# Kernel tuning notes

Hardware: AMD Instinct MI355X
Metric: run time of the kernel (lower is better)

The kernel has to match this reference:

```python
import jax, jax.numpy as jnp
import numpy as np

B, L, HID, H, D = 2, 2048, 1024, 16, 64
ROPE_BASE = 10000.0


def half_rotate(x):
    # [a, b | c, d] -> [-c, -d | a, b] along last dim
    d = x.shape[-1] // 2
    return jnp.concatenate((-x[..., d:], x[..., :d]), axis=-1)


def apply_rope(x, position_ids, base=ROPE_BASE):
    # x: [B, L, H, D]; position_ids: [L] int
    dim = x.shape[-1]
    inv_fre = 1.0 / (base ** (jnp.arange(0, dim, 2, dtype=jnp.float32) / dim))  # [D/2]
    freqs = position_ids.astype(jnp.float32)[None, :, None] * inv_fre  # [1, L, D/2]
    sin = jnp.repeat(jnp.sin(freqs), 2, axis=-1)[:, :, None, :]  # [1, L, 1, D]
    cos = jnp.repeat(jnp.cos(freqs), 2, axis=-1)[:, :, None, :]
    return cos * x + half_rotate(x) * sin


def setup_inputs() -> dict:
    key = jax.random.key(0)
    ks = jax.random.split(key, 5)
    x = jax.random.normal(ks[0], (B, L, HID), dtype=jnp.float32)
    position_id = jnp.arange(L, dtype=jnp.int64)
    # additive causal mask: 0 on/below diagonal, -1e9 above
    causal = jnp.tril(jnp.ones((L, L), dtype=bool))
    atten_mask = jnp.where(causal, 0.0, -1e9).astype(jnp.float32)[None, None]
    s = 1.0 / np.sqrt(HID)
    Wq = jax.random.normal(ks[1], (HID, H * D), dtype=jnp.float32) * s
    Wk = jax.random.normal(ks[2], (HID, H * D), dtype=jnp.float32) * s
    Wv = jax.random.normal(ks[3], (HID, H * D), dtype=jnp.float32) * s
    Wo = jax.random.normal(ks[4], (H * D, HID), dtype=jnp.float32) * s
    return {"x": x, "position_id": position_id, "atten_mask": atten_mask,
            "Wq": Wq, "Wk": Wk, "Wv": Wv, "Wo": Wo}


def reference(x, position_id, atten_mask, Wq, Wk, Wv, Wo):
    b, l, _ = x.shape
    scale = D ** -0.5
    q = (x @ Wq).reshape(b, l, H, D)
    k = (x @ Wk).reshape(b, l, H, D)
    v = (x @ Wv).reshape(b, l, H, D)
    q = apply_rope(q, position_id)
    k = apply_rope(k, position_id)
    # [B, H, Lq, Lk]
    scores = jnp.einsum('bqhd,bkhd->bhqk', q, k) * scale + atten_mask
    attn = jax.nn.softmax(scores.astype(jnp.float32), axis=-1).astype(q.dtype)
    out = jnp.einsum('bhqk,bkhd->bqhd', attn, v).reshape(b, l, H * D)
    return out @ Wo
```

## Files before the change

### kernel.cpp

```cpp
#include <hip/hip_runtime.h>

typedef unsigned short u16;
typedef unsigned int u32;
typedef __attribute__((ext_vector_type(8))) short short8;
typedef __attribute__((ext_vector_type(4))) float f32x4;

#define H_ 16
#define L_ 2048
#define D_ 64
#define HID_ 1024

__device__ __forceinline__ u16 f2bf(float f) {
  union { float f; u32 u; } v; v.f = f;
  u32 r = v.u + 0x7FFFu + ((v.u >> 16) & 1u);
  return (u16)(r >> 16);
}

__device__ __forceinline__ void gl16(const u16* g, u16* l) {
  __builtin_amdgcn_global_load_lds(
      (const __attribute__((address_space(1))) void*)g,
      (__attribute__((address_space(3))) void*)l, 16, 0, 0);
}


__global__ __launch_bounds__(256) void prep_k(
    const float* __restrict__ x, u16* __restrict__ xbf,
    const float* __restrict__ Wq, const float* __restrict__ Wk,
    const float* __restrict__ Wv, const float* __restrict__ Wo,
    u16* __restrict__ dWq, u16* __restrict__ dWk,
    u16* __restrict__ dWv, u16* __restrict__ dWo,
    const int* __restrict__ pos, float2* __restrict__ tab)
{
  __shared__ float t[32][33];
  int blk = blockIdx.x;
  if (blk < 2048) {
    int i = (blk * 256 + threadIdx.x) * 8;
    float4 a = *(const float4*)(x + i);
    float4 b = *(const float4*)(x + i + 4);
    u16 r[8] = { f2bf(a.x), f2bf(a.y), f2bf(a.z), f2bf(a.w),
                 f2bf(b.x), f2bf(b.y), f2bf(b.z), f2bf(b.w) };
    *(uint4*)(xbf + i) = *(const uint4*)r;
  } else if (blk < 6144) {
    int bb = blk - 2048;
    int w = bb >> 10;
    const float* in = (w == 0) ? Wq : (w == 1) ? Wk : (w == 2) ? Wv : Wo;
    u16* out = (w == 0) ? dWq : (w == 1) ? dWk : (w == 2) ? dWv : dWo;
    int bx = bb & 31, by = (bb >> 5) & 31;
    int c = threadIdx.x & 31, r0 = threadIdx.x >> 5;
#pragma unroll
    for (int p = 0; p < 4; ++p) {
      int r = r0 + p * 8;
      t[r][c] = in[(size_t)(by * 32 + r) * 1024 + bx * 32 + c];
    }
    __syncthreads();
#pragma unroll
    for (int p = 0; p < 4; ++p) {
      int r = r0 + p * 8;
      out[(size_t)(bx * 32 + r) * 1024 + by * 32 + c] = f2bf(t[c][r]);
    }
  } else {
    int gid = (blk - 6144) * 256 + threadIdx.x;
    int l = gid >> 5, i = gid & 31;
    float p = (float)pos[l];
    float inv = expf(-((float)(2 * i) / 64.0f) * logf(10000.0f));
    float th = p * inv;
    tab[gid] = make_float2(cosf(th), sinf(th));
  }
}


__global__ __launch_bounds__(256) void qkv_gemm_k(
    const u16* __restrict__ A, const u16* __restrict__ Bt,
    u16* __restrict__ Qo, u16* __restrict__ Ko, u16* __restrict__ Vo,
    const float2* __restrict__ rope)
{
  const int K = 1024;
  __shared__ alignas(16) u16 As[2][8192];
  __shared__ alignas(16) u16 Bs[2][12288];
  int tid = threadIdx.x;
  int orig = blockIdx.x;
  int xcd = orig & 7, idx = orig >> 3;
  int px = xcd & 1, py = xcd >> 1;
  int tn = px * 8 + (idx & 7);
  int tm = py * 8 + (idx >> 3);
  int m0 = tm * 128, n0 = tn * 192;
  int prow = tid >> 3;
  int pB = (tid & 7) ^ (prow & 7);
  const u16* gA0 = A + (size_t)(m0 + prow) * K + pB * 8;
  const u16* gB0 = Bt + (size_t)(n0 + prow) * K + pB * 8;
  int wid = tid >> 6, lane = tid & 63, ln = lane & 15, kg = lane >> 4;
  int wm = wid * 32;
  f32x4 acc[2][12] = {};
  int sw0 = (kg ^ (ln & 7)) * 8;
  int sw1 = ((4 + kg) ^ (ln & 7)) * 8;

  auto stage = [&](int kt, int buf) {
#pragma unroll
    for (int s = 0; s < 4; ++s)
      gl16(gA0 + (size_t)s * 32 * K + kt * 64, &As[buf][s * 2048 + tid * 8]);
#pragma unroll
    for (int s = 0; s < 6; ++s)
      gl16(gB0 + (size_t)s * 32 * K + kt * 64, &Bs[buf][s * 2048 + tid * 8]);
  };

  stage(0, 0);
  int cur = 0;
  for (int kt = 0; kt < 16; ++kt) {
    __builtin_amdgcn_s_barrier();
    if (kt + 1 < 16) {
      stage(kt + 1, cur ^ 1);
      asm volatile("s_waitcnt vmcnt(10)" ::: "memory");
    } else {
      asm volatile("s_waitcnt vmcnt(0)" ::: "memory");
    }
    __builtin_amdgcn_sched_barrier(0);
#pragma unroll
    for (int kk = 0; kk < 2; ++kk) {
      int sw = kk ? sw1 : sw0;
      short8 af0 = *(const short8*)&As[cur][(wm + ln) * 64 + sw];
      short8 af1 = *(const short8*)&As[cur][(wm + 16 + ln) * 64 + sw];
#pragma unroll
      for (int nb = 0; nb < 3; ++nb) {
        short8 bq0 = *(const short8*)&Bs[cur][((nb * 64 + 0) + ln) * 64 + sw];
        short8 bq1 = *(const short8*)&Bs[cur][((nb * 64 + 16) + ln) * 64 + sw];
        short8 bq2 = *(const short8*)&Bs[cur][((nb * 64 + 32) + ln) * 64 + sw];
        short8 bq3 = *(const short8*)&Bs[cur][((nb * 64 + 48) + ln) * 64 + sw];
        acc[0][nb * 4 + 0] = __builtin_amdgcn_mfma_f32_16x16x32_bf16(af0, bq0, acc[0][nb * 4 + 0], 0, 0, 0);
        acc[1][nb * 4 + 0] = __builtin_amdgcn_mfma_f32_16x16x32_bf16(af1, bq0, acc[1][nb * 4 + 0], 0, 0, 0);
        acc[0][nb * 4 + 1] = __builtin_amdgcn_mfma_f32_16x16x32_bf16(af0, bq1, acc[0][nb * 4 + 1], 0, 0, 0);
        acc[1][nb * 4 + 1] = __builtin_amdgcn_mfma_f32_16x16x32_bf16(af1, bq1, acc[1][nb * 4 + 1], 0, 0, 0);
        acc[0][nb * 4 + 2] = __builtin_amdgcn_mfma_f32_16x16x32_bf16(af0, bq2, acc[0][nb * 4 + 2], 0, 0, 0);
        acc[1][nb * 4 + 2] = __builtin_amdgcn_mfma_f32_16x16x32_bf16(af1, bq2, acc[1][nb * 4 + 2], 0, 0, 0);
        acc[0][nb * 4 + 3] = __builtin_amdgcn_mfma_f32_16x16x32_bf16(af0, bq3, acc[0][nb * 4 + 3], 0, 0, 0);
        acc[1][nb * 4 + 3] = __builtin_amdgcn_mfma_f32_16x16x32_bf16(af1, bq3, acc[1][nb * 4 + 3], 0, 0, 0);
      }
    }
    cur ^= 1;
  }

#pragma unroll
  for (int hh = 0; hh < 3; ++hh) {
    int gc0 = n0 + hh * 64;
    int sec = gc0 >> 10;
    int h = (gc0 & 1023) >> 6;
    if (sec < 2) {
      u16* Out = (sec == 0) ? Qo : Ko;
      float sc = (sec == 0) ? 0.180336880f : 1.0f;
#pragma unroll
      for (int mi = 0; mi < 2; ++mi)
#pragma unroll
        for (int j = 0; j < 4; ++j) {
          int mm = m0 + wm + mi * 16 + kg * 4 + j;
          int l = mm & (L_ - 1), bb = mm >> 11;
          const float2* tl = rope + l * 32;
#pragma unroll
          for (int g = 0; g < 2; ++g) {
            int dA = g * 16 + ln;
            float xa = acc[mi][hh * 4 + g][j], xb = acc[mi][hh * 4 + g + 2][j];
            float2 fA = tl[dA >> 1];
            float2 fB = tl[16 + (dA >> 1)];
            float oA = (fA.x * xa - fA.y * xb) * sc;
            float oB = (fB.x * xb + fB.y * xa) * sc;
            size_t base = ((size_t)(bb * H_ + h) * L_ + l) * D_;
            Out[base + dA] = f2bf(oA);
            Out[base + dA + 32] = f2bf(oB);
          }
        }
    } else {
#pragma unroll
      for (int mi = 0; mi < 2; ++mi)
#pragma unroll
        for (int j = 0; j < 4; ++j) {
          int mm = m0 + wm + mi * 16 + kg * 4 + j;
          int l = mm & (L_ - 1), bb = mm >> 11;
          int m = l & 31;
          int sp = ((m >> 2) & 3) * 8 + ((m >> 4) & 1) * 4 + (m & 3);
          size_t base = (size_t)(bb * H_ + h) * (L_ * D_) + (size_t)(l >> 5) * 2048 + sp;
#pragma unroll
          for (int g = 0; g < 4; ++g) {
            int d = g * 16 + ln;
            Vo[base + (size_t)d * 32] = f2bf(acc[mi][hh * 4 + g][j]);
          }
        }
    }
  }
}


__global__ __launch_bounds__(256) void oproj_k(
    const u16* __restrict__ A, const u16* __restrict__ Bt, float* __restrict__ Out)
{
  const int K = 1024;
  __shared__ alignas(16) u16 As[2][4096];
  __shared__ alignas(16) u16 Bs[2][8192];
  int tid = threadIdx.x;
  int orig = blockIdx.x;
  int xcd = orig & 7, idx = orig >> 3;
  int px = xcd & 1, py = xcd >> 1;
  int tn = px * 4 + (idx & 3);
  int tm = py * 16 + (idx >> 2);
  int m0 = tm * 64, n0 = tn * 128;
  int prow = tid >> 3;
  int pB = (tid & 7) ^ (prow & 7);
  const u16* gA0 = A + (size_t)(m0 + prow) * K + pB * 8;
  const u16* gB0 = Bt + (size_t)(n0 + prow) * K + pB * 8;
  int wid = tid >> 6, lane = tid & 63, ln = lane & 15, kg = lane >> 4;
  int wm = (wid >> 1) * 32, wn = (wid & 1) * 64;
  f32x4 acc[2][4] = {};
  int sw0 = (kg ^ (ln & 7)) * 8;
  int sw1 = ((4 + kg) ^ (ln & 7)) * 8;

  auto stage = [&](int kt, int buf) {
#pragma unroll
    for (int s = 0; s < 2; ++s)
      gl16(gA0 + (size_t)s * 32 * K + kt * 64, &As[buf][s * 2048 + tid * 8]);
#pragma unroll
    for (int s = 0; s < 4; ++s)
      gl16(gB0 + (size_t)s * 32 * K + kt * 64, &Bs[buf][s * 2048 + tid * 8]);
  };

  stage(0, 0);
  int cur = 0;
  for (int kt = 0; kt < 16; ++kt) {
    __builtin_amdgcn_s_barrier();
    if (kt + 1 < 16) {
      stage(kt + 1, cur ^ 1);
      asm volatile("s_waitcnt vmcnt(6)" ::: "memory");
    } else {
      asm volatile("s_waitcnt vmcnt(0)" ::: "memory");
    }
    __builtin_amdgcn_sched_barrier(0);
#pragma unroll
    for (int kk = 0; kk < 2; ++kk) {
      int sw = kk ? sw1 : sw0;
      short8 af[2], bfr[4];
#pragma unroll
      for (int i = 0; i < 2; ++i) af[i] = *(const short8*)&As[cur][(wm + i * 16 + ln) * 64 + sw];
#pragma unroll
      for (int i = 0; i < 4; ++i) bfr[i] = *(const short8*)&Bs[cur][(wn + i * 16 + ln) * 64 + sw];
#pragma unroll
      for (int mi = 0; mi < 2; ++mi)
#pragma unroll
        for (int ni = 0; ni < 4; ++ni)
          acc[mi][ni] = __builtin_amdgcn_mfma_f32_16x16x32_bf16(af[mi], bfr[ni], acc[mi][ni], 0, 0, 0);
    }
    cur ^= 1;
  }
#pragma unroll
  for (int mi = 0; mi < 2; ++mi)
#pragma unroll
    for (int j = 0; j < 4; ++j) {
      int mm = m0 + wm + mi * 16 + kg * 4 + j;
#pragma unroll
      for (int ni = 0; ni < 4; ++ni)
        Out[(size_t)mm * 1024 + n0 + wn + ni * 16 + ln] = acc[mi][ni][j];
    }
}

__global__ __launch_bounds__(256) void attn_k(
    const u16* __restrict__ Q, const u16* __restrict__ K,
    const u16* __restrict__ V, u16* __restrict__ AO)
{
  __shared__ alignas(16) u16 Ks[2][8192];
  __shared__ alignas(16) u16 Vs[2][8192];
  int tid = threadIdx.x;
  int wid = tid >> 6, lane = tid & 63;
  int ln = lane & 15, kg = lane >> 4;
  int orig = blockIdx.x;
  int swz = (orig & 7) * 64 + (orig >> 3);
  int bh = swz >> 4;
  int i = swz & 15;
  int tA = i, tB = 31 - i;
  int nA = (tA >> 1) + 1;
  int nB = (tB >> 1) + 1;
  const int NCH = 17;
  int q0A = tA * 64 + wid * 16;
  int q0B = tB * 64 + wid * 16;
  const u16* Qh = Q + (size_t)bh * L_ * D_;
  const u16* Kh = K + (size_t)bh * L_ * D_;
  const u16* Vt = V + (size_t)bh * L_ * D_;

  int srow = tid >> 3, sblk = tid & 7;
  const u16* kb = Kh + (size_t)srow * 64 + ((sblk ^ (srow & 7)) << 3);
  const u16* vb = Vt + (size_t)(tid >> 2) * 32 + (((tid & 3) ^ ((tid >> 3) & 3)) << 3);

  short8 qfA0 = *(const short8*)(Qh + (size_t)(q0A + ln) * D_ + kg * 8);
  short8 qfA1 = *(const short8*)(Qh + (size_t)(q0A + ln) * D_ + 32 + kg * 8);
  short8 qfB0 = *(const short8*)(Qh + (size_t)(q0B + ln) * D_ + kg * 8);
  short8 qfB1 = *(const short8*)(Qh + (size_t)(q0B + ln) * D_ + 32 + kg * 8);

  f32x4 oA[4] = {}, oB[4] = {};
  float lsA = 0.f, lsB = 0.f;
  int sw0 = (kg ^ (ln & 7)) * 8;
  int sw1 = ((4 + kg) ^ (ln & 7)) * 8;
  int vsw = (kg ^ ((ln >> 1) & 3)) * 8;
  int jdA = (tA & 1) * 4 + wid;
  int jdB = (tB & 1) * 4 + wid;

  auto stage = [&](int chunk, int buf) {
    const u16* kc = kb + (size_t)chunk * 8192;
    const u16* vc = vb + (size_t)chunk * 8192;
#pragma unroll
    for (int s2 = 0; s2 < 4; ++s2) {
      gl16(kc + s2 * 2048, &Ks[buf][s2 * 2048 + tid * 8]);
      gl16(vc + s2 * 2048, &Vs[buf][s2 * 2048 + tid * 8]);
    }
  };
  auto seq = [&](int c) { return (c < nA) ? c : c - nA; };

  auto step = [&](int cur, int jd, short8 qf0, short8 qf1,
                  float& lsum, f32x4 (&o)[4]) {
    f32x4 s[8];
    __builtin_amdgcn_s_setprio(1);
#pragma unroll
    for (int j = 0; j < 8; ++j) {
      short8 ka = *(const short8*)&Ks[cur][(j * 16 + ln) * 64 + sw0];
      short8 kc = *(const short8*)&Ks[cur][(j * 16 + ln) * 64 + sw1];
      f32x4 t = {};
      t = __builtin_amdgcn_mfma_f32_16x16x32_bf16(ka, qf0, t, 0, 0, 0);
      t = __builtin_amdgcn_mfma_f32_16x16x32_bf16(kc, qf1, t, 0, 0, 0);
      s[j] = t;
    }
    __builtin_amdgcn_s_setprio(0);
    if (jd < 8) {
#pragma unroll
      for (int j = 0; j < 8; ++j)
#pragma unroll
        for (int r = 0; r < 4; ++r) {
          bool kill = (j > jd) | ((j == jd) & ((kg * 4 + r) > ln));
          if (kill) s[j][r] = -1e30f;
        }
    }
    float ps = 0.f;
    u32 wA[8], wB[8];
#pragma unroll
    for (int j = 0; j < 8; ++j) {
      float p0, p1, p2, p3;
      asm("v_exp_f32 %0, %1" : "=v"(p0) : "v"(s[j][0]));
      asm("v_exp_f32 %0, %1" : "=v"(p1) : "v"(s[j][1]));
      asm("v_exp_f32 %0, %1" : "=v"(p2) : "v"(s[j][2]));
      asm("v_exp_f32 %0, %1" : "=v"(p3) : "v"(s[j][3]));
      ps += (p0 + p1) + (p2 + p3);
      asm("v_cvt_pk_bf16_f32 %0, %1, %2" : "=v"(wA[j]) : "v"(p0), "v"(p1));
      asm("v_cvt_pk_bf16_f32 %0, %1, %2" : "=v"(wB[j]) : "v"(p2), "v"(p3));
    }
    lsum += ps;
#pragma unroll
    for (int g = 0; g < 4; ++g) {
      union { u32 u[4]; short8 s8; } pu;
      pu.u[0] = wA[2 * g];
      pu.u[1] = wB[2 * g];
      pu.u[2] = wA[2 * g + 1];
      pu.u[3] = wB[2 * g + 1];
      short8 vf0 = *(const short8*)&Vs[cur][g * 2048 + ln * 32 + vsw];
      short8 vf1 = *(const short8*)&Vs[cur][g * 2048 + (16 + ln) * 32 + vsw];
      short8 vf2 = *(const short8*)&Vs[cur][g * 2048 + (32 + ln) * 32 + vsw];
      short8 vf3 = *(const short8*)&Vs[cur][g * 2048 + (48 + ln) * 32 + vsw];
      __builtin_amdgcn_s_setprio(1);
      o[0] = __builtin_amdgcn_mfma_f32_16x16x32_bf16(vf0, pu.s8, o[0], 0, 0, 0);
      o[1] = __builtin_amdgcn_mfma_f32_16x16x32_bf16(vf1, pu.s8, o[1], 0, 0, 0);
      o[2] = __builtin_amdgcn_mfma_f32_16x16x32_bf16(vf2, pu.s8, o[2], 0, 0, 0);
      o[3] = __builtin_amdgcn_mfma_f32_16x16x32_bf16(vf3, pu.s8, o[3], 0, 0, 0);
      __builtin_amdgcn_s_setprio(0);
    }
  };

  stage(seq(0), 0);
  int cur = 0;

  for (int c = 0; c < NCH; ++c) {
    __builtin_amdgcn_s_barrier();
    if (c + 1 < NCH) {
      stage(seq(c + 1), cur ^ 1);
      asm volatile("s_waitcnt vmcnt(8)" ::: "memory");
    } else {
      asm volatile("s_waitcnt vmcnt(0)" ::: "memory");
    }
    __builtin_amdgcn_sched_barrier(0);

    if (c < nA) {
      step(cur, (c == nA - 1) ? jdA : 8, qfA0, qfA1, lsA, oA);
    } else {
      int cl = c - nA;
      step(cur, (cl == nB - 1) ? jdB : 8, qfB0, qfB1, lsB, oB);
    }
    cur ^= 1;
  }

  int b = bh >> 4, h = bh & 15;
  lsA += __shfl_xor(lsA, 16);
  lsA += __shfl_xor(lsA, 32);
  lsB += __shfl_xor(lsB, 16);
  lsB += __shfl_xor(lsB, 32);
  float invA = 1.0f / lsA, invB = 1.0f / lsB;
  u16* rowA = AO + ((size_t)(b * L_ + q0A + ln) * H_ + h) * D_;
  u16* rowB = AO + ((size_t)(b * L_ + q0B + ln) * H_ + h) * D_;
#pragma unroll
  for (int dt = 0; dt < 4; ++dt) {
    union { u16 pk[4]; uint2 v; } uA, uB;
#pragma unroll
    for (int r = 0; r < 4; ++r) {
      uA.pk[r] = f2bf(oA[dt][r] * invA);
      uB.pk[r] = f2bf(oB[dt][r] * invB);
    }
    *(uint2*)(rowA + dt * 16 + kg * 4) = uA.v;
    *(uint2*)(rowB + dt * 16 + kg * 4) = uB.v;
  }
}


extern "C" void kernel_launch(void* const* d_in, const int* in_sizes, int n_in,
                              void* d_out, int out_size, void* d_ws, size_t ws_size,
                              hipStream_t stream) {
  (void)in_sizes; (void)n_in; (void)out_size; (void)ws_size;
  const float* x   = (const float*)d_in[0];
  const int*   pos = (const int*)d_in[1];
  const float* Wq  = (const float*)d_in[3];
  const float* Wk  = (const float*)d_in[4];
  const float* Wv  = (const float*)d_in[5];
  const float* Wo  = (const float*)d_in[6];

  char* ws = (char*)d_ws;
  u16* xbf = (u16*)ws;
  u16* Wt3 = (u16*)(ws + (size_t)( 8 << 20));
  u16* Wto = (u16*)(ws + (size_t)(14 << 20));
  u16* Qb  = (u16*)(ws + (size_t)(16 << 20));
  u16* Kb  = (u16*)(ws + (size_t)(24 << 20));
  u16* Vt  = (u16*)(ws + (size_t)(32 << 20));
  u16* AO  = (u16*)(ws + (size_t)(40 << 20));
  float2* tab = (float2*)(ws + (size_t)(48 << 20));

  prep_k<<<6400, 256, 0, stream>>>(
      x, xbf, Wq, Wk, Wv, Wo,
      Wt3, Wt3 + (size_t)1048576, Wt3 + (size_t)2097152, Wto, pos, tab);
  qkv_gemm_k<<<512, 256, 0, stream>>>(xbf, Wt3, Qb, Kb, Vt, tab);
  attn_k<<<512, 256, 0, stream>>>(Qb, Kb, Vt, AO);
  oproj_k<<<512, 256, 0, stream>>>(AO, Wto, (float*)d_out);
}
```

Baseline: 94.71 us.

## Use 2x2 warp tiling in QKV GEMM with LDS exchange for split RoPE head

Changes the QKV projection kernel's warp layout from 4 warps each covering 32 rows by 192 columns to a 2x2 grid where each warp covers 64 rows by 96 columns. Each k-step now needs 10 LDS fragment loads instead of 14 for the same 24 MFMAs, which cuts shared-memory read traffic. Because the middle head's 64 columns are now split across two warps, RoPE needs the partner half, so the accumulators are exchanged through LDS after the main loop. This adds two barriers and an extra LDS write/read in the epilogue.

```diff
diff --git a/kernel.cpp b/kernel.cpp
--- a/kernel.cpp
+++ b/kernel.cpp
@@ -89,8 +89,9 @@
   const u16* gA0 = A + (size_t)(m0 + prow) * K + pB * 8;
   const u16* gB0 = Bt + (size_t)(n0 + prow) * K + pB * 8;
   int wid = tid >> 6, lane = tid & 63, ln = lane & 15, kg = lane >> 4;
-  int wm = wid * 32;
-  f32x4 acc[2][12] = {};
+  int wr = wid >> 1, wc = wid & 1;
+  int wm = wr * 64, wn2 = wc * 96;
+  f32x4 acc[4][6] = {};
   int sw0 = (kg ^ (ln & 7)) * 8;
   int sw1 = ((4 + kg) ^ (ln & 7)) * 8;
 
@@ -117,58 +118,72 @@
 #pragma unroll
     for (int kk = 0; kk < 2; ++kk) {
       int sw = kk ? sw1 : sw0;
-      short8 af0 = *(const short8*)&As[cur][(wm + ln) * 64 + sw];
-      short8 af1 = *(const short8*)&As[cur][(wm + 16 + ln) * 64 + sw];
-#pragma unroll
-      for (int nb = 0; nb < 3; ++nb) {
-        short8 bq0 = *(const short8*)&Bs[cur][((nb * 64 + 0) + ln) * 64 + sw];
-        short8 bq1 = *(const short8*)&Bs[cur][((nb * 64 + 16) + ln) * 64 + sw];
-        short8 bq2 = *(const short8*)&Bs[cur][((nb * 64 + 32) + ln) * 64 + sw];
-        short8 bq3 = *(const short8*)&Bs[cur][((nb * 64 + 48) + ln) * 64 + sw];
-        acc[0][nb * 4 + 0] = __builtin_amdgcn_mfma_f32_16x16x32_bf16(af0, bq0, acc[0][nb * 4 + 0], 0, 0, 0);
-        acc[1][nb * 4 + 0] = __builtin_amdgcn_mfma_f32_16x16x32_bf16(af1, bq0, acc[1][nb * 4 + 0], 0, 0, 0);
-        acc[0][nb * 4 + 1] = __builtin_amdgcn_mfma_f32_16x16x32_bf16(af0, bq1, acc[0][nb * 4 + 1], 0, 0, 0);
-        acc[1][nb * 4 + 1] = __builtin_amdgcn_mfma_f32_16x16x32_bf16(af1, bq1, acc[1][nb * 4 + 1], 0, 0, 0);
-        acc[0][nb * 4 + 2] = __builtin_amdgcn_mfma_f32_16x16x32_bf16(af0, bq2, acc[0][nb * 4 + 2], 0, 0, 0);
-        acc[1][nb * 4 + 2] = __builtin_amdgcn_mfma_f32_16x16x32_bf16(af1, bq2, acc[1][nb * 4 + 2], 0, 0, 0);
-        acc[0][nb * 4 + 3] = __builtin_amdgcn_mfma_f32_16x16x32_bf16(af0, bq3, acc[0][nb * 4 + 3], 0, 0, 0);
-        acc[1][nb * 4 + 3] = __builtin_amdgcn_mfma_f32_16x16x32_bf16(af1, bq3, acc[1][nb * 4 + 3], 0, 0, 0);
-      }
+      short8 af[4], bf[6];
+#pragma unroll
+      for (int i = 0; i < 4; ++i)
+        af[i] = *(const short8*)&As[cur][(wm + i * 16 + ln) * 64 + sw];
+#pragma unroll
+      for (int g = 0; g < 6; ++g)
+        bf[g] = *(const short8*)&Bs[cur][(wn2 + g * 16 + ln) * 64 + sw];
+#pragma unroll
+      for (int g = 0; g < 6; ++g)
+#pragma unroll
+        for (int i = 0; i < 4; ++i)
+          acc[i][g] = __builtin_amdgcn_mfma_f32_16x16x32_bf16(af[i], bf[g], acc[i][g], 0, 0, 0);
     }
     cur ^= 1;
   }
 
-#pragma unroll
-  for (int hh = 0; hh < 3; ++hh) {
+  __syncthreads();
+  f32x4* xch = (f32x4*)(&As[0][0]);
+  {
+    int xbase = ((wr * 2 + wc) * 2) * 4 * 64;
+#pragma unroll
+    for (int g2 = 0; g2 < 2; ++g2)
+#pragma unroll
+      for (int mi = 0; mi < 4; ++mi)
+        xch[xbase + (g2 * 4 + mi) * 64 + lane] = acc[mi][wc ? g2 : 4 + g2];
+  }
+  __syncthreads();
+  f32x4 part[2][4];
+  {
+    int pbase = ((wr * 2 + (wc ^ 1)) * 2) * 4 * 64;
+#pragma unroll
+    for (int g2 = 0; g2 < 2; ++g2)
+#pragma unroll
+      for (int mi = 0; mi < 4; ++mi)
+        part[g2][mi] = xch[pbase + (g2 * 4 + mi) * 64 + lane];
+  }
+
+  {
+    int hh = wc ? 2 : 0;
+    int gb = wc ? 2 : 0;
     int gc0 = n0 + hh * 64;
-    int sec = gc0 >> 10;
-    int h = (gc0 & 1023) >> 6;
+    int sec = gc0 >> 10, h = (gc0 & 1023) >> 6;
     if (sec < 2) {
       u16* Out = (sec == 0) ? Qo : Ko;
       float sc = (sec == 0) ? 0.180336880f : 1.0f;
 #pragma unroll
-      for (int mi = 0; mi < 2; ++mi)
+      for (int mi = 0; mi < 4; ++mi)
 #pragma unroll
         for (int j = 0; j < 4; ++j) {
           int mm = m0 + wm + mi * 16 + kg * 4 + j;
           int l = mm & (L_ - 1), bb = mm >> 11;
           const float2* tl = rope + l * 32;
-#pragma unroll
-          for (int g = 0; g < 2; ++g) {
-            int dA = g * 16 + ln;
-            float xa = acc[mi][hh * 4 + g][j], xb = acc[mi][hh * 4 + g + 2][j];
+          size_t base = ((size_t)(bb * H_ + h) * L_ + l) * D_;
+#pragma unroll
+          for (int g2 = 0; g2 < 2; ++g2) {
+            int dA = g2 * 16 + ln;
+            float xa = acc[mi][gb + g2][j], xb = acc[mi][gb + g2 + 2][j];
             float2 fA = tl[dA >> 1];
             float2 fB = tl[16 + (dA >> 1)];
-            float oA = (fA.x * xa - fA.y * xb) * sc;
-            float oB = (fB.x * xb + fB.y * xa) * sc;
-            size_t base = ((size_t)(bb * H_ + h) * L_ + l) * D_;
-            Out[base + dA] = f2bf(oA);
-            Out[base + dA + 32] = f2bf(oB);
+            Out[base + dA] = f2bf((fA.x * xa - fA.y * xb) * sc);
+            Out[base + dA + 32] = f2bf((fB.x * xb + fB.y * xa) * sc);
           }
         }
     } else {
 #pragma unroll
-      for (int mi = 0; mi < 2; ++mi)
+      for (int mi = 0; mi < 4; ++mi)
 #pragma unroll
         for (int j = 0; j < 4; ++j) {
           int mm = m0 + wm + mi * 16 + kg * 4 + j;
@@ -177,9 +192,56 @@
           int sp = ((m >> 2) & 3) * 8 + ((m >> 4) & 1) * 4 + (m & 3);
           size_t base = (size_t)(bb * H_ + h) * (L_ * D_) + (size_t)(l >> 5) * 2048 + sp;
 #pragma unroll
-          for (int g = 0; g < 4; ++g) {
-            int d = g * 16 + ln;
-            Vo[base + (size_t)d * 32] = f2bf(acc[mi][hh * 4 + g][j]);
+          for (int g2 = 0; g2 < 4; ++g2) {
+            int d = g2 * 16 + ln;
+            Vo[base + (size_t)d * 32] = f2bf(acc[mi][gb + g2][j]);
+          }
+        }
+    }
+  }
+
+  {
+    int gc0 = n0 + 64;
+    int sec = gc0 >> 10, h = (gc0 & 1023) >> 6;
+    if (sec < 2) {
+      u16* Out = (sec == 0) ? Qo : Ko;
+      float sc = (sec == 0) ? 0.180336880f : 1.0f;
+#pragma unroll
+      for (int mi = 0; mi < 4; ++mi)
+#pragma unroll
+        for (int j = 0; j < 4; ++j) {
+          int mm = m0 + wm + mi * 16 + kg * 4 + j;
+          int l = mm & (L_ - 1), bb = mm >> 11;
+          const float2* tl = rope + l * 32;
+          size_t base = ((size_t)(bb * H_ + h) * L_ + l) * D_;
+#pragma unroll
+          for (int g2 = 0; g2 < 2; ++g2) {
+            int dA = g2 * 16 + ln;
+            float2 fA = tl[dA >> 1];
+            float2 fB = tl[16 + (dA >> 1)];
+            if (wc == 0) {
+              float xa = acc[mi][4 + g2][j], xb = part[g2][mi][j];
+              Out[base + dA] = f2bf((fA.x * xa - fA.y * xb) * sc);
+            } else {
+              float xb = acc[mi][g2][j], xa = part[g2][mi][j];
+              Out[base + dA + 32] = f2bf((fB.x * xb + fB.y * xa) * sc);
+            }
+          }
+        }
+    } else {
+#pragma unroll
+      for (int mi = 0; mi < 4; ++mi)
+#pragma unroll
+        for (int j = 0; j < 4; ++j) {
+          int mm = m0 + wm + mi * 16 + kg * 4 + j;
+          int l = mm & (L_ - 1), bb = mm >> 11;
+          int m = l & 31;
+          int sp = ((m >> 2) & 3) * 8 + ((m >> 4) & 1) * 4 + (m & 3);
+          size_t base = (size_t)(bb * H_ + h) * (L_ * D_) + (size_t)(l >> 5) * 2048 + sp;
+#pragma unroll
+          for (int g2 = 0; g2 < 2; ++g2) {
+            int d = (wc ? 32 : 0) + g2 * 16 + ln;
+            Vo[base + (size_t)d * 32] = f2bf(acc[mi][wc ? g2 : 4 + g2][j]);
           }
         }
     }
```

New measurement: 159.7 us. 1.69x slower.
